# Kernel tuning notes

Measured on AMD Instinct MI355X. Metric: run time of the kernel, lower is better.

The kernel has to match this reference:

```python
import jax, jax.numpy as jnp
import numpy as np

B, CIN, H, W = 8, 4, 512, 512
HID, NCLS = 32, 19
WIN = 3
SCALE = 2


def conv(x, w, b, stride):
    # torch Conv2d(kernel=3, padding=1, stride=stride) equivalent
    y = jax.lax.conv_general_dilated(
        x, w, (stride, stride), [(1, 1), (1, 1)],
        dimension_numbers=('NCHW', 'OIHW', 'NCHW'))
    return y + b[None, :, None, None]


def interp_matrix(n_in, n_out, dtype):
    # 1D bilinear interpolation matrix, align_corners=True semantics
    pos = jnp.arange(n_out, dtype=dtype) * ((n_in - 1) / (n_out - 1))
    lo = jnp.clip(jnp.floor(pos).astype(jnp.int32), 0, n_in - 2)
    frac = pos - lo.astype(dtype)
    M = jnp.zeros((n_out, n_in), dtype)
    M = M.at[jnp.arange(n_out), lo].add(1 - frac)
    M = M.at[jnp.arange(n_out), lo + 1].add(frac)
    return M


def setup_inputs() -> dict:
    key = jax.random.key(0)
    ks = jax.random.split(key, 3)
    x = jax.random.normal(ks[0], (B, CIN, H, W), jnp.float32)
    w1 = jax.random.normal(ks[1], (HID, CIN, 3, 3), jnp.float32) * 0.1
    b1 = jnp.zeros((HID,), jnp.float32)
    w2 = jax.random.normal(ks[2], (NCLS, HID, 3, 3), jnp.float32) * 0.1
    b2 = jnp.zeros((NCLS,), jnp.float32)
    return {"x": x, "w1": w1, "b1": b1, "w2": w2, "b2": b2}


def reference(x, w1, b1, w2, b2):
    # --- cnn backbone -> class response maps ---
    h = jax.nn.relu(conv(x, w1, b1, 2))          # [B, HID, H/2, W/2]
    cmaps = conv(h, w2, b2, 1)                   # [B, NCLS, H/2, W/2]

    # --- bilinear upsample, align_corners=True (scale_factor=2) ---
    hi, wi = cmaps.shape[2], cmaps.shape[3]
    Mh = interp_matrix(hi, hi * SCALE, cmaps.dtype)
    Mw = interp_matrix(wi, wi * SCALE, cmaps.dtype)
    cmaps = jnp.einsum('oh,bchw,pw->bcop', Mh, cmaps, Mw)  # [B, NCLS, H, W]

    # --- peak stimulation: 3x3 local-max with -inf padding ---
    neg_inf = jnp.asarray(-jnp.inf, cmaps.dtype)
    local_max = jax.lax.reduce_window(
        cmaps, neg_inf, jax.lax.max,
        (1, 1, WIN, WIN), (1, 1, 1, 1),
        [(0, 0), (0, 0), (1, 1), (1, 1)])

    # median filter: per-(batch, class) spatial median threshold
    med = jnp.median(cmaps.reshape(cmaps.shape[0], cmaps.shape[1], -1), axis=2)
    med = med[:, :, None, None]

    peak_map = (cmaps == local_max) & (cmaps >= med)       # bool peak mask
    pf = peak_map.astype(cmaps.dtype)

    # aggregation: mean of map values at peaks -> class logits [B, NCLS]
    logits = (cmaps * pf).sum(axis=(2, 3)) / pf.sum(axis=(2, 3))
    return cmaps, logits
```

## Files before the change

### kernel.cpp

```cpp
#include <hip/hip_runtime.h>

#define B_ 8
#define CIN_ 4
#define H_ 512
#define W_ 512
#define HID_ 32
#define NCLS_ 19
#define HO_ 256
#define WO_ 256
#define UP_ 512
#define NPLANE (B_*NCLS_)
#define PLANE_ELEMS (UP_*UP_)
#define KMED1 131071u


__device__ __forceinline__ unsigned f2key(float f) {
  unsigned u = __float_as_uint(f);
  return (u & 0x80000000u) ? ~u : (u | 0x80000000u);
}
__device__ __forceinline__ float key2f(unsigned k) {
  unsigned u = (k & 0x80000000u) ? (k & 0x7FFFFFFFu) : ~k;
  return __uint_as_float(u);
}
__device__ __forceinline__ float ninf() { return __uint_as_float(0xFF800000u); }

__device__ __forceinline__ float up_val(const float* __restrict__ p, int oy, int ox) {
  const float s = (float)(255.0 / 511.0);
  float posy = (float)oy * s;
  int ly = (int)posy; if (ly > 254) ly = 254;
  float fy = posy - (float)ly;
  float posx = (float)ox * s;
  int lx = (int)posx; if (lx > 254) lx = 254;
  float fx = posx - (float)lx;
  const float* q = p + ly * WO_ + lx;
  float a = q[0], b = q[1], c = q[WO_], d = q[WO_ + 1];
  float r0 = fmaf(fx, b - a, a);
  float r1 = fmaf(fx, d - c, c);
  return fmaf(fy, r1 - r0, r0);
}

__global__ __launch_bounds__(256, 4) void conv1_kernel(
    const float* __restrict__ x, const float* __restrict__ w1,
    const float* __restrict__ b1, float* __restrict__ h) {
  int t = threadIdx.x & 63;
  int r = threadIdx.x >> 6;
  int oh = blockIdx.x * 4 + r;
  int b  = blockIdx.z;
  int ow0 = blockIdx.y * 128 + t * 2;
  int ic0 = 2 * ow0;

  float2 acc[HID_];
  #pragma unroll
  for (int oc = 0; oc < HID_; ++oc) {
    float bb = b1[oc];
    acc[oc].x = bb; acc[oc].y = bb;
  }

  #pragma unroll
  for (int ci = 0; ci < CIN_; ++ci) {
    const float* xp = x + ((size_t)(b * CIN_ + ci)) * H_ * W_;
    float4 A0, A1, A2;
    float lm[3];
    #pragma unroll
    for (int kh = 0; kh < 3; ++kh) {
      int ih = 2 * oh + kh - 1;
      float4 Av; float lv = 0.f;
      if ((unsigned)ih < (unsigned)H_) {
        const float* row = xp + ih * W_;
        Av = *reinterpret_cast<const float4*>(row + ic0);
        lv = (ic0 > 0) ? row[ic0 - 1] : 0.f;
      } else {
        Av.x = 0.f; Av.y = 0.f; Av.z = 0.f; Av.w = 0.f;
      }
      if (kh == 0) A0 = Av; else if (kh == 1) A1 = Av; else A2 = Av;
      lm[kh] = lv;
    }
    #pragma unroll
    for (int oc = 0; oc < HID_; ++oc) {
      const float* wp = w1 + ((size_t)oc * CIN_ + ci) * 9;
      {
        float w0 = wp[0], w1v = wp[1], w2v = wp[2];
        acc[oc].x += w0 * lm[0] + w1v * A0.x + w2v * A0.y;
        acc[oc].y += w0 * A0.y  + w1v * A0.z + w2v * A0.w;
      }
      {
        float w0 = wp[3], w1v = wp[4], w2v = wp[5];
        acc[oc].x += w0 * lm[1] + w1v * A1.x + w2v * A1.y;
        acc[oc].y += w0 * A1.y  + w1v * A1.z + w2v * A1.w;
      }
      {
        float w0 = wp[6], w1v = wp[7], w2v = wp[8];
        acc[oc].x += w0 * lm[2] + w1v * A2.x + w2v * A2.y;
        acc[oc].y += w0 * A2.y  + w1v * A2.z + w2v * A2.w;
      }
    }
  }
  #pragma unroll
  for (int oc = 0; oc < HID_; ++oc) {
    float2 o;
    o.x = fmaxf(acc[oc].x, 0.f); o.y = fmaxf(acc[oc].y, 0.f);
    *reinterpret_cast<float2*>(h + (((size_t)(b * HID_ + oc) * HO_ + oh) * WO_ + ow0)) = o;
  }
}

__global__ __launch_bounds__(256, 4) void conv2_kernel(
    const float* __restrict__ h, const float* __restrict__ w2,
    const float* __restrict__ b2, float* __restrict__ c0) {
  int t = threadIdx.x & 63;
  int r = threadIdx.x >> 6;
  int oh = blockIdx.x * 4 + r;
  int b  = blockIdx.z;
  int ow0 = blockIdx.y * 128 + t * 2;

  float2 acc[NCLS_];
  #pragma unroll
  for (int oc = 0; oc < NCLS_; ++oc) {
    float bb = b2[oc];
    acc[oc].x = bb; acc[oc].y = bb;
  }

  for (int ci = 0; ci < HID_; ++ci) {
    const float* hp = h + ((size_t)(b * HID_ + ci)) * HO_ * WO_;
    float2 M0, M1, M2;
    float L[3], R[3];
    #pragma unroll
    for (int kh = 0; kh < 3; ++kh) {
      int ih = oh + kh - 1;
      float2 Mv;
      float lv = 0.f, rv = 0.f;
      if ((unsigned)ih < (unsigned)HO_) {
        const float* row = hp + ih * WO_;
        Mv = *reinterpret_cast<const float2*>(row + ow0);
        lv = (ow0 > 0) ? row[ow0 - 1] : 0.f;
        rv = (ow0 + 2 < WO_) ? row[ow0 + 2] : 0.f;
      } else {
        Mv.x = 0.f; Mv.y = 0.f;
      }
      if (kh == 0) M0 = Mv; else if (kh == 1) M1 = Mv; else M2 = Mv;
      L[kh] = lv; R[kh] = rv;
    }
    const float* wpc = w2 + ci * 9;
    #pragma unroll
    for (int oc = 0; oc < NCLS_; ++oc) {
      const float* wp = wpc + oc * (HID_ * 9);
      {
        float w0 = wp[0], w1v = wp[1], w2v = wp[2];
        acc[oc].x += w0 * L[0]  + w1v * M0.x + w2v * M0.y;
        acc[oc].y += w0 * M0.x + w1v * M0.y + w2v * R[0];
      }
      {
        float w0 = wp[3], w1v = wp[4], w2v = wp[5];
        acc[oc].x += w0 * L[1]  + w1v * M1.x + w2v * M1.y;
        acc[oc].y += w0 * M1.x + w1v * M1.y + w2v * R[1];
      }
      {
        float w0 = wp[6], w1v = wp[7], w2v = wp[8];
        acc[oc].x += w0 * L[2]  + w1v * M2.x + w2v * M2.y;
        acc[oc].y += w0 * M2.x + w1v * M2.y + w2v * R[2];
      }
    }
  }
  #pragma unroll
  for (int oc = 0; oc < NCLS_; ++oc) {
    *reinterpret_cast<float2*>(c0 + (((size_t)(b * NCLS_ + oc) * HO_ + oh) * WO_ + ow0)) = acc[oc];
  }
}

__global__ __launch_bounds__(256) void upsample_hist_kernel(
    const float* __restrict__ c0, float* __restrict__ out,
    unsigned* __restrict__ ghist) {
  __shared__ unsigned lh[4 * 2048];
  int tid = threadIdx.x;
  int chunk = blockIdx.x;
  int plane = blockIdx.y;
  unsigned* mylh = lh + ((tid >> 6) << 11);
  for (int i = tid; i < 4 * 2048; i += 256) lh[i] = 0u;
  __syncthreads();
  const float* p = c0 + (size_t)plane * HO_ * WO_;
  float* op = out + (size_t)plane * PLANE_ELEMS;
  int ox0 = (tid & 127) * 4;
  #pragma unroll 2
  for (int it = 0; it < 32; ++it) {
    int oy = chunk * 64 + it * 2 + (tid >> 7);
    float4 o;
    o.x = up_val(p, oy, ox0 + 0);
    o.y = up_val(p, oy, ox0 + 1);
    o.z = up_val(p, oy, ox0 + 2);
    o.w = up_val(p, oy, ox0 + 3);
    *reinterpret_cast<float4*>(op + (size_t)oy * UP_ + ox0) = o;
    atomicAdd(&mylh[f2key(o.x) >> 21], 1u);
    atomicAdd(&mylh[f2key(o.y) >> 21], 1u);
    atomicAdd(&mylh[f2key(o.z) >> 21], 1u);
    atomicAdd(&mylh[f2key(o.w) >> 21], 1u);
  }
  __syncthreads();
  for (int i = tid; i < 2048; i += 256) {
    unsigned c = lh[i] + lh[2048 + i] + lh[4096 + i] + lh[6144 + i];
    if (c) atomicAdd(&ghist[(size_t)plane * 2048 + i], c);
  }
}


__global__ void init_kernel(unsigned* kArr, unsigned* pvalArr, unsigned* gbArr,
                            unsigned* flagArr) {
  int i = threadIdx.x;
  if (i < NPLANE) { kArr[i] = KMED1; pvalArr[i] = 0u; gbArr[i] = 0u; flagArr[i] = 0u; }
}

__global__ __launch_bounds__(256) void hist_pass_kernel(
    const float* __restrict__ up, const unsigned* __restrict__ pvalArr,
    unsigned* __restrict__ ghist, int shift, unsigned bmask, unsigned fmask) {
  __shared__ unsigned lh[4 * 2048];
  int tid = threadIdx.x;
  int chunk = blockIdx.x;
  int plane = blockIdx.y;
  unsigned* mylh = lh + ((tid >> 6) << 11);
  for (int i = tid; i < 4 * 2048; i += 256) lh[i] = 0u;
  __syncthreads();
  unsigned fval = pvalArr[plane] & fmask;
  const float4* p4 = reinterpret_cast<const float4*>(up + (size_t)plane * PLANE_ELEMS)
                     + (size_t)chunk * 8192;
  #pragma unroll 4
  for (int it = 0; it < 32; ++it) {
    float4 v = p4[it * 256 + tid];
    unsigned k0 = f2key(v.x), k1 = f2key(v.y), k2 = f2key(v.z), k3 = f2key(v.w);
    if ((k0 & fmask) == fval) atomicAdd(&mylh[(k0 >> shift) & bmask], 1u);
    if ((k1 & fmask) == fval) atomicAdd(&mylh[(k1 >> shift) & bmask], 1u);
    if ((k2 & fmask) == fval) atomicAdd(&mylh[(k2 >> shift) & bmask], 1u);
    if ((k3 & fmask) == fval) atomicAdd(&mylh[(k3 >> shift) & bmask], 1u);
  }
  __syncthreads();
  for (int i = tid; i < 2048; i += 256) {
    unsigned c = lh[i] + lh[2048 + i] + lh[4096 + i] + lh[6144 + i];
    if (c) atomicAdd(&ghist[(size_t)plane * 2048 + i], c);
  }
}

__global__ __launch_bounds__(256) void select_kernel(
    unsigned* __restrict__ ghist, unsigned* kArr, unsigned* pvalArr, unsigned* gbArr,
    unsigned* v1Arr, unsigned* v2Arr, unsigned* flagArr,
    int shift, unsigned bmask, int nbins, int last) {
  __shared__ unsigned ssum[256], stmp[256];
  __shared__ unsigned sBin, sBelow, sCand[256];
  int tid = threadIdx.x;
  int plane = blockIdx.x;
  unsigned* hp = ghist + (size_t)plane * 2048;
  unsigned k = kArr[plane];
  unsigned lv[8];
  int b0 = tid * 8;
  unsigned lsum = 0;
  #pragma unroll
  for (int j = 0; j < 8; ++j) {
    unsigned c = (b0 + j < nbins) ? hp[b0 + j] : 0u;
    lv[j] = c; lsum += c;
  }
  ssum[tid] = lsum;
  __syncthreads();
  for (int off = 1; off < 256; off <<= 1) {
    stmp[tid] = (tid >= off) ? ssum[tid - off] : 0u; __syncthreads();
    ssum[tid] += stmp[tid]; __syncthreads();
  }
  unsigned incl = ssum[tid], excl = incl - lsum;
  if (excl <= k && k < incl) {
    unsigned kk = k - excl, below = excl;
    #pragma unroll
    for (int j = 0; j < 8; ++j) {
      if (kk < lv[j]) { sBin = (unsigned)(b0 + j); sBelow = below; break; }
      kk -= lv[j]; below += lv[j];
    }
  }
  __syncthreads();
  unsigned bin = sBin, below = sBelow;
  unsigned pvalNew = pvalArr[plane] | (bin << shift);
  unsigned gbNew = gbArr[plane] + below;
  if (!last) {
    for (int i = tid; i < 2048; i += 256) hp[i] = 0u;
    if (tid == 0) { kArr[plane] = k - below; pvalArr[plane] = pvalNew; gbArr[plane] = gbNew; }
  } else {
    unsigned cand = 0xFFFFFFFFu;
    #pragma unroll
    for (int j = 0; j < 8; ++j) {
      int g = b0 + j;
      if (g > (int)bin && g < nbins && lv[j] > 0u && (unsigned)g < cand) cand = (unsigned)g;
    }
    sCand[tid] = cand;
    __syncthreads();
    for (int s = 128; s > 0; s >>= 1) {
      if (tid < s) { unsigned o = sCand[tid + s]; if (o < sCand[tid]) sCand[tid] = o; }
      __syncthreads();
    }
    if (tid == 0) {
      unsigned ceq = hp[bin];
      v1Arr[plane] = pvalNew;
      if (131072u < gbNew + ceq) {
        v2Arr[plane] = pvalNew; flagArr[plane] = 0u;
      } else if (sCand[0] != 0xFFFFFFFFu) {
        v2Arr[plane] = (pvalNew & ~(bmask << shift)) | (sCand[0] << shift);
        flagArr[plane] = 0u;
      } else {
        v2Arr[plane] = 0xFFFFFFFFu; flagArr[plane] = 1u;
      }
    }
  }
}

__global__ __launch_bounds__(256) void minabove_kernel(
    const float* __restrict__ up, const unsigned* __restrict__ flagArr,
    const unsigned* __restrict__ v1Arr, unsigned* __restrict__ v2Arr) {
  int plane = blockIdx.y, chunk = blockIdx.x, tid = threadIdx.x;
  if (!flagArr[plane]) return;
  unsigned v1 = v1Arr[plane];
  const float4* base = reinterpret_cast<const float4*>(up + (size_t)plane * PLANE_ELEMS)
                       + (size_t)chunk * 4096;
  unsigned m = 0xFFFFFFFFu;
  for (int it = 0; it < 16; ++it) {
    float4 v = base[it * 256 + tid];
    unsigned k;
    k = f2key(v.x); if (k > v1 && k < m) m = k;
    k = f2key(v.y); if (k > v1 && k < m) m = k;
    k = f2key(v.z); if (k > v1 && k < m) m = k;
    k = f2key(v.w); if (k > v1 && k < m) m = k;
  }
  for (int off = 32; off > 0; off >>= 1) {
    unsigned o = __shfl_down(m, off, 64);
    if (o < m) m = o;
  }
  if ((tid & 63) == 0) atomicMin(&v2Arr[plane], m);
}

__global__ void finalize_kernel(const unsigned* __restrict__ v1Arr,
                                const unsigned* __restrict__ v2Arr,
                                float* __restrict__ med) {
  int i = threadIdx.x;
  if (i < NPLANE) med[i] = 0.5f * (key2f(v1Arr[i]) + key2f(v2Arr[i]));
}

__device__ __forceinline__ void row_load(const float* __restrict__ p, int y, int x0,
                                         float4& v, float& l, float& r) {
  if ((unsigned)y >= (unsigned)UP_) {
    float ni = ninf();
    v.x = v.y = v.z = v.w = ni; l = ni; r = ni;
    return;
  }
  const float* row = p + y * UP_ + x0;
  v = *reinterpret_cast<const float4*>(row);
  l = (x0 > 0) ? row[-1] : ninf();
  r = (x0 < UP_ - 4) ? row[4] : ninf();
}
__device__ __forceinline__ float4 hmax4(const float4& v, float l, float r) {
  float4 h;
  h.x = fmaxf(fmaxf(l, v.x), v.y);
  h.y = fmaxf(fmaxf(v.x, v.y), v.z);
  h.z = fmaxf(fmaxf(v.y, v.z), v.w);
  h.w = fmaxf(fmaxf(v.z, v.w), r);
  return h;
}

__global__ __launch_bounds__(256) void peak2_kernel(
    const float* __restrict__ cm, const float* __restrict__ med_arr,
    float* __restrict__ sums, float* __restrict__ cnts) {
  int tid = threadIdx.x;
  int plane = blockIdx.x;
  int strip = tid & 127;
  int ychunk = blockIdx.y * 2 + (tid >> 7);
  int x0 = strip * 4;
  int ystart = ychunk * 64;
  const float* p = cm + (size_t)plane * PLANE_ELEMS;
  float med = med_arr[plane];

  float4 v, vn; float l, r;
  row_load(p, ystart - 1, x0, v, l, r);
  float4 hprev = hmax4(v, l, r);
  row_load(p, ystart, x0, v, l, r);
  float4 hcur = hmax4(v, l, r);
  float4 vcur = v;

  float lsum = 0.f; int lcnt = 0;
  for (int yi = 0; yi < 64; ++yi) {
    int y = ystart + yi;
    float ln, rn;
    row_load(p, y + 1, x0, vn, ln, rn);
    float4 hnext = hmax4(vn, ln, rn);
    float mx = fmaxf(fmaxf(hprev.x, hcur.x), hnext.x);
    float my = fmaxf(fmaxf(hprev.y, hcur.y), hnext.y);
    float mz = fmaxf(fmaxf(hprev.z, hcur.z), hnext.z);
    float mw = fmaxf(fmaxf(hprev.w, hcur.w), hnext.w);
    if (vcur.x == mx && vcur.x >= med) { lsum += vcur.x; ++lcnt; }
    if (vcur.y == my && vcur.y >= med) { lsum += vcur.y; ++lcnt; }
    if (vcur.z == mz && vcur.z >= med) { lsum += vcur.z; ++lcnt; }
    if (vcur.w == mw && vcur.w >= med) { lsum += vcur.w; ++lcnt; }
    hprev = hcur; hcur = hnext; vcur = vn;
  }

  __shared__ float ss[256];
  __shared__ int sc[256];
  ss[tid] = lsum; sc[tid] = lcnt;
  __syncthreads();
  for (int s = 128; s > 0; s >>= 1) {
    if (tid < s) { ss[tid] += ss[tid + s]; sc[tid] += sc[tid + s]; }
    __syncthreads();
  }
  if (tid == 0) {
    atomicAdd(&sums[plane], ss[0]);
    atomicAdd(&cnts[plane], (float)sc[0]);
  }
}

__global__ void logits_kernel(const float* __restrict__ sums,
                              const float* __restrict__ cnts,
                              float* __restrict__ out) {
  int i = threadIdx.x;
  if (i < NPLANE) out[i] = sums[i] / cnts[i];
}

extern "C" void kernel_launch(void* const* d_in, const int* in_sizes, int n_in,
                              void* d_out, int out_size, void* d_ws, size_t ws_size,
                              hipStream_t stream) {
  const float* x  = (const float*)d_in[0];
  const float* w1 = (const float*)d_in[1];
  const float* b1 = (const float*)d_in[2];
  const float* w2 = (const float*)d_in[3];
  const float* b2 = (const float*)d_in[4];
  float* out = (float*)d_out;

  float* ws = (float*)d_ws;
  float* c0 = ws;
  unsigned* hist    = (unsigned*)(ws + 9961472);
  unsigned* kArr    = hist + 311296;
  unsigned* pvalArr = kArr + NPLANE;
  unsigned* gbArr   = pvalArr + NPLANE;
  unsigned* v1Arr   = gbArr + NPLANE;
  unsigned* v2Arr   = v1Arr + NPLANE;
  unsigned* flagArr = v2Arr + NPLANE;
  float* med  = (float*)(flagArr + NPLANE);
  float* sums = med + NPLANE;
  float* cnts = sums + NPLANE;
  float* h = out;

  init_kernel<<<1, 256, 0, stream>>>(kArr, pvalArr, gbArr, flagArr);
  hipMemsetAsync(hist, 0, (size_t)NPLANE * 2048 * sizeof(unsigned), stream);
  hipMemsetAsync(sums, 0, 2 * NPLANE * sizeof(float), stream);

  conv1_kernel<<<dim3(64, 2, 8), 256, 0, stream>>>(x, w1, b1, h);
  conv2_kernel<<<dim3(64, 2, 8), 256, 0, stream>>>(h, w2, b2, c0);

  upsample_hist_kernel<<<dim3(8, NPLANE), 256, 0, stream>>>(c0, out, hist);
  select_kernel<<<dim3(NPLANE), 256, 0, stream>>>(hist, kArr, pvalArr, gbArr,
      v1Arr, v2Arr, flagArr, 21, 0x7FFu, 2048, 0);
  hist_pass_kernel<<<dim3(8, NPLANE), 256, 0, stream>>>(out, pvalArr, hist, 10, 0x7FFu, 0xFFE00000u);
  select_kernel<<<dim3(NPLANE), 256, 0, stream>>>(hist, kArr, pvalArr, gbArr,
      v1Arr, v2Arr, flagArr, 10, 0x7FFu, 2048, 0);
  hist_pass_kernel<<<dim3(8, NPLANE), 256, 0, stream>>>(out, pvalArr, hist, 0, 0x3FFu, 0xFFFFFC00u);
  select_kernel<<<dim3(NPLANE), 256, 0, stream>>>(hist, kArr, pvalArr, gbArr,
      v1Arr, v2Arr, flagArr, 0, 0x3FFu, 1024, 1);
  minabove_kernel<<<dim3(16, NPLANE), 256, 0, stream>>>(out, flagArr, v1Arr, v2Arr);
  finalize_kernel<<<1, 256, 0, stream>>>(v1Arr, v2Arr, med);

  peak2_kernel<<<dim3(NPLANE, 4), 256, 0, stream>>>(out, med, sums, cnts);
  logits_kernel<<<1, 192, 0, stream>>>(sums, cnts, out + (out_size - NPLANE));
}
```

Measured before the change: 503.0 us.

## Stage conv2 input halo tiles in double-buffered shared memory

```diff
diff --git a/kernel.cpp b/kernel.cpp
--- a/kernel.cpp
+++ b/kernel.cpp
@@ -106,11 +106,29 @@
 __global__ __launch_bounds__(256, 4) void conv2_kernel(
     const float* __restrict__ h, const float* __restrict__ w2,
     const float* __restrict__ b2, float* __restrict__ c0) {
-  int t = threadIdx.x & 63;
-  int r = threadIdx.x >> 6;
+  __shared__ float sh[2][6][132];
+
+  int tid = threadIdx.x;
+  int t = tid & 63;
+  int r = tid >> 6;
   int oh = blockIdx.x * 4 + r;
   int b  = blockIdx.z;
-  int ow0 = blockIdx.y * 128 + t * 2;
+  int owb = blockIdx.y * 128;
+  int ow0 = owb + t * 2;
+  int ih0 = blockIdx.x * 4 - 1;
+
+  int srow[4], scol[4];
+  bool sval[4];
+  #pragma unroll
+  for (int s = 0; s < 4; ++s) {
+    int idx = tid + 256 * s;
+    int rw = idx / 132;
+    int cl = idx - rw * 132;
+    srow[s] = rw; scol[s] = cl;
+    int gr = ih0 + rw;
+    int gc = owb - 1 + cl;
+    sval[s] = (idx < 792) && ((unsigned)gr < (unsigned)HO_) && ((unsigned)gc < (unsigned)WO_);
+  }
 
   float2 acc[NCLS_];
   #pragma unroll
@@ -119,26 +137,50 @@
     acc[oc].x = bb; acc[oc].y = bb;
   }
 
+  const size_t plane = (size_t)HO_ * WO_;
+  const float* hb = h + (size_t)b * HID_ * plane;
+
+  {
+    const float* hp = hb;
+    #pragma unroll
+    for (int s = 0; s < 4; ++s) {
+      int idx = tid + 256 * s;
+      if (idx < 792) {
+        float v = 0.f;
+        if (sval[s]) v = hp[(ih0 + srow[s]) * WO_ + (owb - 1 + scol[s])];
+        sh[0][srow[s]][scol[s]] = v;
+      }
+    }
+  }
+  __syncthreads();
+
   for (int ci = 0; ci < HID_; ++ci) {
-    const float* hp = h + ((size_t)(b * HID_ + ci)) * HO_ * WO_;
+    int cur = ci & 1;
+    if (ci + 1 < HID_) {
+      const float* hp = hb + (size_t)(ci + 1) * plane;
+      #pragma unroll
+      for (int s = 0; s < 4; ++s) {
+        int idx = tid + 256 * s;
+        if (idx < 792) {
+          float v = 0.f;
+          if (sval[s]) v = hp[(ih0 + srow[s]) * WO_ + (owb - 1 + scol[s])];
+          sh[cur ^ 1][srow[s]][scol[s]] = v;
+        }
+      }
+    }
+
     float2 M0, M1, M2;
     float L[3], R[3];
-    #pragma unroll
-    for (int kh = 0; kh < 3; ++kh) {
-      int ih = oh + kh - 1;
-      float2 Mv;
-      float lv = 0.f, rv = 0.f;
-      if ((unsigned)ih < (unsigned)HO_) {
-        const float* row = hp + ih * WO_;
-        Mv = *reinterpret_cast<const float2*>(row + ow0);
-        lv = (ow0 > 0) ? row[ow0 - 1] : 0.f;
-        rv = (ow0 + 2 < WO_) ? row[ow0 + 2] : 0.f;
-      } else {
-        Mv.x = 0.f; Mv.y = 0.f;
-      }
-      if (kh == 0) M0 = Mv; else if (kh == 1) M1 = Mv; else M2 = Mv;
-      L[kh] = lv; R[kh] = rv;
-    }
+    {
+      const float* row0 = &sh[cur][r + 0][0];
+      const float* row1 = &sh[cur][r + 1][0];
+      const float* row2 = &sh[cur][r + 2][0];
+      int c = 2 * t;
+      L[0] = row0[c]; M0.x = row0[c + 1]; M0.y = row0[c + 2]; R[0] = row0[c + 3];
+      L[1] = row1[c]; M1.x = row1[c + 1]; M1.y = row1[c + 2]; R[1] = row1[c + 3];
+      L[2] = row2[c]; M2.x = row2[c + 1]; M2.y = row2[c + 2]; R[2] = row2[c + 3];
+    }
+
     const float* wpc = w2 + ci * 9;
     #pragma unroll
     for (int oc = 0; oc < NCLS_; ++oc) {
@@ -159,7 +201,9 @@
         acc[oc].y += w0 * M2.x + w1v * M2.y + w2v * R[2];
       }
     }
-  }
+    __syncthreads();
+  }
+
   #pragma unroll
   for (int oc = 0; oc < NCLS_; ++oc) {
     *reinterpret_cast<float2*>(c0 + (((size_t)(b * NCLS_ + oc) * HO_ + oh) * WO_ + ow0)) = acc[oc];
```

After: 568.7 us. 13.1% more time.
